# Kernel tuning notes

Hardware: AMD Instinct MI355X
Metric: run time of the kernel (lower is better)

## Reference

```python
import jax, jax.numpy as jnp
import numpy as np

NUM_HEADS = 16
D_MODEL = 1024
DEPTH = D_MODEL // NUM_HEADS
B, S = 4, 1024  # q,k seq len = S; v seq len = S-1


def setup_inputs() -> dict:
    key = jax.random.key(0)
    ks = jax.random.split(key, 6)
    scale = 1.0 / np.sqrt(D_MODEL)
    return {
        "v": jax.random.normal(ks[0], (B, S - 1, D_MODEL), dtype=jnp.float32),
        "k": jax.random.normal(ks[1], (B, S, D_MODEL), dtype=jnp.float32),
        "q": jax.random.normal(ks[2], (B, S, D_MODEL), dtype=jnp.float32),
        "mask": jnp.zeros((B, S - 1, S - 1), dtype=jnp.float32),
        "Wv": jax.random.normal(ks[3], (D_MODEL, D_MODEL), dtype=jnp.float32) * scale,
        "bv": jnp.zeros((D_MODEL,), dtype=jnp.float32),
        "Wd": jax.random.normal(ks[4], (D_MODEL, D_MODEL), dtype=jnp.float32) * scale,
        "bd": jnp.zeros((D_MODEL,), dtype=jnp.float32),
    }


def _split_heads(x):
    # (B, T, d_model) -> (B, H, T, depth)
    b, t, _ = x.shape
    return x.reshape(b, t, NUM_HEADS, DEPTH).transpose(0, 2, 1, 3)


def reference(v, k, q, mask, Wv, bv, Wd, bd):
    # 3-D q/k path: qq=q, kk=k (q_layers/k_layers/wq/wk unused)
    vv = v @ Wv + bv                       # (B, S-1, d_model)
    qh = _split_heads(q)                   # (B, H, S, depth)
    kh = _split_heads(k)                   # (B, H, S, depth)
    vh = _split_heads(vv)                  # (B, H, S-1, depth)

    scores = jnp.einsum('bhqd,bhkd->bhqk', qh, kh)      # (B, H, S, S)
    scores = scores[:, :, 1:, :-1]                      # (B, H, S-1, S-1)
    dk = jnp.asarray(DEPTH, scores.dtype)
    nl = jax.nn.relu(scores / jnp.sqrt(dk))
    nl = nl + mask[:, None, :, :] * (-1e9)
    att = jax.nn.softmax(nl, axis=-1)                   # (B, H, S-1, S-1)

    out = jnp.einsum('bhqk,bhkd->bhqd', att, vh)        # (B, H, S-1, depth)
    out = out.transpose(0, 2, 1, 3).reshape(v.shape[0], -1, D_MODEL)  # (B, S-1, d_model)
    output = out @ Wd + bd
    return output, att
```

## Files before the change

### kernel.cpp

```cpp
#include <hip/hip_runtime.h>
#include <hip/hip_bf16.h>

#define NUM_HEADS 16
#define DM 1024
#define DEPTH 64
#define BB 4
#define SS 1024
#define SL 1023
#define M_ROWS (BB*SL)

typedef __attribute__((ext_vector_type(8))) short short8;
typedef __attribute__((ext_vector_type(4))) float floatx4;

__device__ inline unsigned short f2bf(float f) {
  __hip_bfloat16 hb = __float2bfloat16(f);
  return *reinterpret_cast<unsigned short*>(&hb);
}
__device__ inline short8 ld_frag(const unsigned short* p) {
  return *reinterpret_cast<const short8*>(p);
}

template <bool A_BF16, bool OUT_BF16>
__global__ __launch_bounds__(256) void gemm_bias(
    const void* __restrict__ Av, const float* __restrict__ B,
    const float* __restrict__ bias, void* __restrict__ Cv, int M)
{
  __shared__ unsigned short bshT[128][40];
  const int tid = threadIdx.x;
  const int w = tid >> 6, lane = tid & 63, q4 = lane >> 4, l16 = lane & 15;
  const int wm = w >> 1, wn = w & 1;
  const int rb = blockIdx.y * 128 + wm * 64;
  const int cb = blockIdx.x * 128;
  const int wc = wn * 64;

  floatx4 acc[4][4];
  #pragma unroll
  for (int i = 0; i < 4; i++)
    #pragma unroll
    for (int j = 0; j < 4; j++) acc[i][j] = (floatx4){0.f,0.f,0.f,0.f};

  const int sn = tid & 127;
  const int sk = (tid >> 7) * 16;

  for (int k0 = 0; k0 < DM; k0 += 32) {
    __syncthreads();
    {
      const float* bp = B + (size_t)(k0 + sk) * DM + cb + sn;
      unsigned short tmp[16];
      #pragma unroll
      for (int j = 0; j < 16; j++) tmp[j] = f2bf(bp[(size_t)j * DM]);
      *(uint4*)&bshT[sn][sk]     = *(uint4*)&tmp[0];
      *(uint4*)&bshT[sn][sk + 8] = *(uint4*)&tmp[8];
    }
    __syncthreads();

    short8 af[4];
    #pragma unroll
    for (int i = 0; i < 4; i++) {
      int m = rb + i * 16 + l16;
      if (m < M) {
        if (A_BF16) {
          af[i] = ld_frag((const unsigned short*)Av + (size_t)m * DM + k0 + q4 * 8);
        } else {
          const float* ap = (const float*)Av + (size_t)m * DM + k0 + q4 * 8;
          float4 f0 = *(const float4*)ap;
          float4 f1 = *(const float4*)(ap + 4);
          short8 t;
          t[0]=f2bf(f0.x); t[1]=f2bf(f0.y); t[2]=f2bf(f0.z); t[3]=f2bf(f0.w);
          t[4]=f2bf(f1.x); t[5]=f2bf(f1.y); t[6]=f2bf(f1.z); t[7]=f2bf(f1.w);
          af[i] = t;
        }
      } else {
        af[i] = (short8){0,0,0,0,0,0,0,0};
      }
    }
    #pragma unroll
    for (int jn = 0; jn < 4; jn++) {
      short8 bf = ld_frag(&bshT[wc + jn * 16 + l16][q4 * 8]);
      #pragma unroll
      for (int i = 0; i < 4; i++)
        acc[i][jn] = __builtin_amdgcn_mfma_f32_16x16x32_bf16(af[i], bf, acc[i][jn], 0, 0, 0);
    }
  }

  #pragma unroll
  for (int jn = 0; jn < 4; jn++) {
    int col = cb + wc + jn * 16 + l16;
    float bb = bias[col];
    #pragma unroll
    for (int i = 0; i < 4; i++) {
      #pragma unroll
      for (int r = 0; r < 4; r++) {
        int m = rb + i * 16 + q4 * 4 + r;
        if (m < M) {
          float val = acc[i][jn][r] + bb;
          if (OUT_BF16) ((unsigned short*)Cv)[(size_t)m * DM + col] = f2bf(val);
          else          ((float*)Cv)[(size_t)m * DM + col] = val;
        }
      }
    }
  }
}

__global__ __launch_bounds__(256) void attn_kernel(
    const float* __restrict__ Q, const float* __restrict__ Kg,
    const float* __restrict__ Mask, const unsigned short* __restrict__ VV,
    float* __restrict__ Att, unsigned short* __restrict__ Out2)
{
  const int qt = blockIdx.x, h = blockIdx.y, b = blockIdx.z;
  const int tid = threadIdx.x;
  const int w = tid >> 6, lane = tid & 63, q4 = lane >> 4, l16 = lane & 15;
  const int qi0 = qt * 64;
  const int qb = w * 16;

  __shared__ unsigned short qsh[64][72];
  __shared__ unsigned short ksh[64][72];
  __shared__ unsigned short vshT[64][72];
  __shared__ unsigned short psh[4][16][72];

  {
    int qr = tid >> 2, d0 = (tid & 3) * 16;
    int qi = qi0 + qr;
    unsigned short tmp[16];
    if (qi < SL) {
      const float* src = Q + ((size_t)b * SS + qi + 1) * DM + h * DEPTH + d0;
      #pragma unroll
      for (int j = 0; j < 16; j += 4) {
        float4 f = *(const float4*)(src + j);
        tmp[j+0]=f2bf(f.x); tmp[j+1]=f2bf(f.y); tmp[j+2]=f2bf(f.z); tmp[j+3]=f2bf(f.w);
      }
    } else {
      #pragma unroll
      for (int j = 0; j < 16; j++) tmp[j] = 0;
    }
    *(uint4*)&qsh[qr][d0]     = *(uint4*)&tmp[0];
    *(uint4*)&qsh[qr][d0 + 8] = *(uint4*)&tmp[8];
  }

  auto stageK = [&](int kt) {
    int kr = tid >> 2, d0 = (tid & 3) * 16;
    int kj = kt * 64 + kr;
    unsigned short tmp[16];
    if (kj < SL) {
      const float* src = Kg + ((size_t)b * SS + kj) * DM + h * DEPTH + d0;
      #pragma unroll
      for (int j = 0; j < 16; j += 4) {
        float4 f = *(const float4*)(src + j);
        tmp[j+0]=f2bf(f.x); tmp[j+1]=f2bf(f.y); tmp[j+2]=f2bf(f.z); tmp[j+3]=f2bf(f.w);
      }
    } else {
      #pragma unroll
      for (int j = 0; j < 16; j++) tmp[j] = 0;
    }
    *(uint4*)&ksh[kr][d0]     = *(uint4*)&tmp[0];
    *(uint4*)&ksh[kr][d0 + 8] = *(uint4*)&tmp[8];
  };

  auto stageV = [&](int kt) {
    int d = tid & 63, k16 = (tid >> 6) * 16;
    unsigned short tmp[16];
    #pragma unroll
    for (int j = 0; j < 16; j++) {
      int kj = kt * 64 + k16 + j;
      tmp[j] = (kj < SL) ? VV[((size_t)b * SL + kj) * DM + h * DEPTH + d] : (unsigned short)0;
    }
    *(uint4*)&vshT[d][k16]     = *(uint4*)&tmp[0];
    *(uint4*)&vshT[d][k16 + 8] = *(uint4*)&tmp[8];
  };

  __syncthreads();

  float rsv[4] = {0.f, 0.f, 0.f, 0.f};
  for (int kt = 0; kt < 16; kt++) {
    __syncthreads();
    stageK(kt);
    __syncthreads();
    #pragma unroll
    for (int nt = 0; nt < 4; nt++) {
      floatx4 s = (floatx4){0.f,0.f,0.f,0.f};
      s = __builtin_amdgcn_mfma_f32_16x16x32_bf16(
            ld_frag(&qsh[qb + l16][q4*8]), ld_frag(&ksh[nt*16 + l16][q4*8]), s, 0,0,0);
      s = __builtin_amdgcn_mfma_f32_16x16x32_bf16(
            ld_frag(&qsh[qb + l16][32 + q4*8]), ld_frag(&ksh[nt*16 + l16][32 + q4*8]), s, 0,0,0);
      int kj = kt * 64 + nt * 16 + l16;
      bool kv = kj < SL;
      int qi_b = qi0 + qb + q4 * 4;
      const float* mp = Mask + ((size_t)b * SL + qi_b) * SL + kj;
      #pragma unroll
      for (int r = 0; r < 4; r++) {
        int qi = qi_b + r;
        float mval = (kv && qi < SL) ? mp[(size_t)r * SL] : 0.f;
        float sv = fmaxf(s[r] * 0.125f, 0.f) + mval * (-1e9f);
        float p = kv ? __expf(sv) : 0.f;
        rsv[r] += p;
      }
    }
  }
  #pragma unroll
  for (int r = 0; r < 4; r++) {
    #pragma unroll
    for (int off = 1; off < 16; off <<= 1) rsv[r] += __shfl_xor(rsv[r], off, 64);
  }
  float inv[4];
  #pragma unroll
  for (int r = 0; r < 4; r++) inv[r] = 1.f / rsv[r];

  floatx4 oacc[4];
  #pragma unroll
  for (int i = 0; i < 4; i++) oacc[i] = (floatx4){0.f,0.f,0.f,0.f};

  for (int kt = 0; kt < 16; kt++) {
    __syncthreads();
    stageK(kt);
    stageV(kt);
    __syncthreads();
    #pragma unroll
    for (int nt = 0; nt < 4; nt++) {
      floatx4 s = (floatx4){0.f,0.f,0.f,0.f};
      s = __builtin_amdgcn_mfma_f32_16x16x32_bf16(
            ld_frag(&qsh[qb + l16][q4*8]), ld_frag(&ksh[nt*16 + l16][q4*8]), s, 0,0,0);
      s = __builtin_amdgcn_mfma_f32_16x16x32_bf16(
            ld_frag(&qsh[qb + l16][32 + q4*8]), ld_frag(&ksh[nt*16 + l16][32 + q4*8]), s, 0,0,0);
      int kj = kt * 64 + nt * 16 + l16;
      bool kv = kj < SL;
      int qi_b = qi0 + qb + q4 * 4;
      const float* mp = Mask + ((size_t)b * SL + qi_b) * SL + kj;
      #pragma unroll
      for (int r = 0; r < 4; r++) {
        int qi = qi_b + r;
        bool qv = qi < SL;
        float mval = (kv && qv) ? mp[(size_t)r * SL] : 0.f;
        float sv = fmaxf(s[r] * 0.125f, 0.f) + mval * (-1e9f);
        float p = kv ? __expf(sv) : 0.f;
        float pn = p * inv[r];
        if (kv && qv)
          Att[(((size_t)(b * NUM_HEADS + h)) * SL + qi) * SL + kj] = pn;
        psh[w][q4 * 4 + r][nt * 16 + l16] = f2bf(pn);
      }
    }
    short8 pa0 = ld_frag(&psh[w][l16][q4 * 8]);
    short8 pa1 = ld_frag(&psh[w][l16][32 + q4 * 8]);
    #pragma unroll
    for (int nt2 = 0; nt2 < 4; nt2++) {
      oacc[nt2] = __builtin_amdgcn_mfma_f32_16x16x32_bf16(
                    pa0, ld_frag(&vshT[nt2*16 + l16][q4*8]), oacc[nt2], 0,0,0);
      oacc[nt2] = __builtin_amdgcn_mfma_f32_16x16x32_bf16(
                    pa1, ld_frag(&vshT[nt2*16 + l16][32 + q4*8]), oacc[nt2], 0,0,0);
    }
  }

  #pragma unroll
  for (int nt2 = 0; nt2 < 4; nt2++) {
    #pragma unroll
    for (int r = 0; r < 4; r++) {
      int qi = qi0 + qb + q4 * 4 + r;
      if (qi < SL)
        Out2[((size_t)b * SL + qi) * DM + h * DEPTH + nt2 * 16 + l16] = f2bf(oacc[nt2][r]);
    }
  }
}

extern "C" void kernel_launch(void* const* d_in, const int* in_sizes, int n_in,
                              void* d_out, int out_size, void* d_ws, size_t ws_size,
                              hipStream_t stream) {
  const float* v    = (const float*)d_in[0];
  const float* k    = (const float*)d_in[1];
  const float* q    = (const float*)d_in[2];
  const float* mask = (const float*)d_in[3];
  const float* Wv   = (const float*)d_in[4];
  const float* bv   = (const float*)d_in[5];
  const float* Wd   = (const float*)d_in[6];
  const float* bd   = (const float*)d_in[7];

  float* out = (float*)d_out;
  float* att = out + (size_t)M_ROWS * DM;
  unsigned short* vv   = (unsigned short*)d_ws;
  unsigned short* out2 = vv + (size_t)M_ROWS * DM;

  gemm_bias<false, true><<<dim3(DM/128, (M_ROWS+127)/128), 256, 0, stream>>>(
      (const void*)v, Wv, bv, (void*)vv, M_ROWS);
  attn_kernel<<<dim3(16, NUM_HEADS, BB), 256, 0, stream>>>(q, k, mask, vv, att, out2);
  gemm_bias<true, false><<<dim3(DM/128, (M_ROWS+127)/128), 256, 0, stream>>>(
      (const void*)out2, Wd, bd, (void*)out, M_ROWS);
}
```

Baseline: 782.5 us.

## Pre-convert operands to bf16 and double-buffer GEMM tiles via global_load_lds

Adds separate kernels that convert v to bf16 and write transposed bf16 copies of Wv and Wd. The GEMMs then stream both operands into swizzled, double-buffered LDS with direct global-to-LDS loads. This replaces the per-iteration strided fp32 weight loads and in-loop conversions with a smaller 64x128 tile. Scratch buffers borrow the att output area and the vv workspace, which relies on the launch order to stay correct, and the extra launches and conversion passes add memory traffic.

New measurement: 667.0 us. 14.8% less time.

```diff
diff --git a/kernel.cpp b/kernel.cpp
--- a/kernel.cpp
+++ b/kernel.cpp
@@ -20,80 +20,138 @@
   return *reinterpret_cast<const short8*>(p);
 }
 
-template <bool A_BF16, bool OUT_BF16>
-__global__ __launch_bounds__(256) void gemm_bias(
-    const void* __restrict__ Av, const float* __restrict__ B,
-    const float* __restrict__ bias, void* __restrict__ Cv, int M)
+#define GLDS(g, l) __builtin_amdgcn_global_load_lds( \
+    (const __attribute__((address_space(1))) void*)(g), \
+    (__attribute__((address_space(3))) void*)(l), 16, 0, 0)
+
+__global__ __launch_bounds__(256) void f32_to_bf16_vec(
+    const float* __restrict__ in, unsigned short* __restrict__ out, int n8)
 {
-  __shared__ unsigned short bshT[128][40];
+  int i = blockIdx.x * 256 + threadIdx.x;
+  if (i >= n8) return;
+  const float4 f0 = ((const float4*)in)[(size_t)i * 2];
+  const float4 f1 = ((const float4*)in)[(size_t)i * 2 + 1];
+  unsigned short t[8];
+  t[0]=f2bf(f0.x); t[1]=f2bf(f0.y); t[2]=f2bf(f0.z); t[3]=f2bf(f0.w);
+  t[4]=f2bf(f1.x); t[5]=f2bf(f1.y); t[6]=f2bf(f1.z); t[7]=f2bf(f1.w);
+  ((uint4*)out)[i] = *(uint4*)t;
+}
+
+__global__ __launch_bounds__(256) void transpose_to_bf16(
+    const float* __restrict__ W, unsigned short* __restrict__ WT)
+{
+  __shared__ unsigned short tile[64][72];
+  const int tid = threadIdx.x;
+  const int k0 = blockIdx.y * 64, n0 = blockIdx.x * 64;
+  {
+    const int kl = tid >> 2, nc = (tid & 3) * 16;
+    const float* src = W + (size_t)(k0 + kl) * DM + n0 + nc;
+    #pragma unroll
+    for (int j = 0; j < 16; j += 4) {
+      float4 f = *(const float4*)(src + j);
+      tile[nc + j + 0][kl] = f2bf(f.x);
+      tile[nc + j + 1][kl] = f2bf(f.y);
+      tile[nc + j + 2][kl] = f2bf(f.z);
+      tile[nc + j + 3][kl] = f2bf(f.w);
+    }
+  }
+  __syncthreads();
+  {
+    const int nl = tid >> 2, kc = (tid & 3) * 16;
+    unsigned short tmp[16];
+    #pragma unroll
+    for (int j = 0; j < 16; j++) tmp[j] = tile[nl][kc + j];
+    unsigned short* dst = WT + (size_t)(n0 + nl) * DM + k0 + kc;
+    *(uint4*)&dst[0] = *(uint4*)&tmp[0];
+    *(uint4*)&dst[8] = *(uint4*)&tmp[8];
+  }
+}
+
+template <bool OUT_BF16>
+__global__ __launch_bounds__(256) void gemm_bt(
+    const unsigned short* __restrict__ A,
+    const unsigned short* __restrict__ BT,
+    const float* __restrict__ bias,
+    void* __restrict__ Cv, int M)
+{
+  constexpr int BM = 64, BN = 128, BK = 32;
+  __shared__ __align__(16) unsigned short As[2][BM * BK];
+  __shared__ __align__(16) unsigned short Bs[2][BN * BK];
+
   const int tid = threadIdx.x;
   const int w = tid >> 6, lane = tid & 63, q4 = lane >> 4, l16 = lane & 15;
   const int wm = w >> 1, wn = w & 1;
-  const int rb = blockIdx.y * 128 + wm * 64;
-  const int cb = blockIdx.x * 128;
-  const int wc = wn * 64;
-
-  floatx4 acc[4][4];
-  #pragma unroll
-  for (int i = 0; i < 4; i++)
+  const int rb = blockIdx.y * BM;
+  const int cb = blockIdx.x * BN;
+
+  const int a_row = tid >> 2;
+  const int a_slot = (tid & 3) ^ ((a_row >> 1) & 3);
+  int a_grow = rb + a_row; if (a_grow >= M) a_grow = M - 1;
+  const unsigned short* a_src = A + (size_t)a_grow * DM + a_slot * 8;
+  const int b_row0 = tid >> 2;
+  const int b_row1 = 64 + (tid >> 2);
+  const int b_slot0 = (tid & 3) ^ ((b_row0 >> 1) & 3);
+  const int b_slot1 = (tid & 3) ^ ((b_row1 >> 1) & 3);
+  const unsigned short* b_src0 = BT + (size_t)(cb + b_row0) * DM + b_slot0 * 8;
+  const unsigned short* b_src1 = BT + (size_t)(cb + b_row1) * DM + b_slot1 * 8;
+
+  int aoff[2], boff[4];
+  #pragma unroll
+  for (int i = 0; i < 2; i++) {
+    int r = wm * 32 + i * 16 + l16;
+    aoff[i] = r * BK + ((q4 ^ ((r >> 1) & 3)) * 8);
+  }
+  #pragma unroll
+  for (int j = 0; j < 4; j++) {
+    int r = wn * 64 + j * 16 + l16;
+    boff[j] = r * BK + ((q4 ^ ((r >> 1) & 3)) * 8);
+  }
+
+  floatx4 acc[2][4];
+  #pragma unroll
+  for (int i = 0; i < 2; i++)
     #pragma unroll
     for (int j = 0; j < 4; j++) acc[i][j] = (floatx4){0.f,0.f,0.f,0.f};
 
-  const int sn = tid & 127;
-  const int sk = (tid >> 7) * 16;
-
-  for (int k0 = 0; k0 < DM; k0 += 32) {
-    __syncthreads();
-    {
-      const float* bp = B + (size_t)(k0 + sk) * DM + cb + sn;
-      unsigned short tmp[16];
-      #pragma unroll
-      for (int j = 0; j < 16; j++) tmp[j] = f2bf(bp[(size_t)j * DM]);
-      *(uint4*)&bshT[sn][sk]     = *(uint4*)&tmp[0];
-      *(uint4*)&bshT[sn][sk + 8] = *(uint4*)&tmp[8];
-    }
-    __syncthreads();
-
-    short8 af[4];
-    #pragma unroll
-    for (int i = 0; i < 4; i++) {
-      int m = rb + i * 16 + l16;
-      if (m < M) {
-        if (A_BF16) {
-          af[i] = ld_frag((const unsigned short*)Av + (size_t)m * DM + k0 + q4 * 8);
-        } else {
-          const float* ap = (const float*)Av + (size_t)m * DM + k0 + q4 * 8;
-          float4 f0 = *(const float4*)ap;
-          float4 f1 = *(const float4*)(ap + 4);
-          short8 t;
-          t[0]=f2bf(f0.x); t[1]=f2bf(f0.y); t[2]=f2bf(f0.z); t[3]=f2bf(f0.w);
-          t[4]=f2bf(f1.x); t[5]=f2bf(f1.y); t[6]=f2bf(f1.z); t[7]=f2bf(f1.w);
-          af[i] = t;
-        }
-      } else {
-        af[i] = (short8){0,0,0,0,0,0,0,0};
-      }
-    }
-    #pragma unroll
-    for (int jn = 0; jn < 4; jn++) {
-      short8 bf = ld_frag(&bshT[wc + jn * 16 + l16][q4 * 8]);
-      #pragma unroll
-      for (int i = 0; i < 4; i++)
-        acc[i][jn] = __builtin_amdgcn_mfma_f32_16x16x32_bf16(af[i], bf, acc[i][jn], 0, 0, 0);
-    }
-  }
-
-  #pragma unroll
-  for (int jn = 0; jn < 4; jn++) {
-    int col = cb + wc + jn * 16 + l16;
+  GLDS(a_src,  &As[0][tid * 8]);
+  GLDS(b_src0, &Bs[0][tid * 8]);
+  GLDS(b_src1, &Bs[0][2048 + tid * 8]);
+  __syncthreads();
+
+  int cur = 0;
+  constexpr int NT = DM / BK;
+  for (int t = 0; t < NT; ++t) {
+    if (t + 1 < NT) {
+      const int kn = (t + 1) * BK;
+      GLDS(a_src + kn,  &As[cur ^ 1][tid * 8]);
+      GLDS(b_src0 + kn, &Bs[cur ^ 1][tid * 8]);
+      GLDS(b_src1 + kn, &Bs[cur ^ 1][2048 + tid * 8]);
+    }
+    short8 af[2], bfr[4];
+    #pragma unroll
+    for (int i = 0; i < 2; i++) af[i] = ld_frag(&As[cur][aoff[i]]);
+    #pragma unroll
+    for (int j = 0; j < 4; j++) bfr[j] = ld_frag(&Bs[cur][boff[j]]);
+    #pragma unroll
+    for (int i = 0; i < 2; i++)
+      #pragma unroll
+      for (int j = 0; j < 4; j++)
+        acc[i][j] = __builtin_amdgcn_mfma_f32_16x16x32_bf16(af[i], bfr[j], acc[i][j], 0, 0, 0);
+    __syncthreads();
+    cur ^= 1;
+  }
+
+  #pragma unroll
+  for (int j = 0; j < 4; j++) {
+    int col = cb + wn * 64 + j * 16 + l16;
     float bb = bias[col];
     #pragma unroll
-    for (int i = 0; i < 4; i++) {
+    for (int i = 0; i < 2; i++) {
       #pragma unroll
       for (int r = 0; r < 4; r++) {
-        int m = rb + i * 16 + q4 * 4 + r;
+        int m = rb + wm * 32 + i * 16 + q4 * 4 + r;
         if (m < M) {
-          float val = acc[i][jn][r] + bb;
+          float val = acc[i][j][r] + bb;
           if (OUT_BF16) ((unsigned short*)Cv)[(size_t)m * DM + col] = f2bf(val);
           else          ((float*)Cv)[(size_t)m * DM + col] = val;
         }
@@ -277,9 +335,16 @@
   unsigned short* vv   = (unsigned short*)d_ws;
   unsigned short* out2 = vv + (size_t)M_ROWS * DM;
 
-  gemm_bias<false, true><<<dim3(DM/128, (M_ROWS+127)/128), 256, 0, stream>>>(
-      (const void*)v, Wv, bv, (void*)vv, M_ROWS);
+  unsigned short* WvT = (unsigned short*)att;
+  unsigned short* vbf = WvT + (size_t)DM * DM;
+  unsigned short* WdT = vv;
+
+  const int n8 = (M_ROWS * DM) / 8;
+
+  f32_to_bf16_vec<<<dim3((n8 + 255) / 256), 256, 0, stream>>>(v, vbf, n8);
+  transpose_to_bf16<<<dim3(16, 16), 256, 0, stream>>>(Wv, WvT);
+  gemm_bt<true><<<dim3(DM/128, (M_ROWS+63)/64), 256, 0, stream>>>(vbf, WvT, bv, (void*)vv, M_ROWS);
   attn_kernel<<<dim3(16, NUM_HEADS, BB), 256, 0, stream>>>(q, k, mask, vv, att, out2);
-  gemm_bias<true, false><<<dim3(DM/128, (M_ROWS+127)/128), 256, 0, stream>>>(
-      (const void*)out2, Wd, bd, (void*)out, M_ROWS);
-}
+  transpose_to_bf16<<<dim3(16, 16), 256, 0, stream>>>(Wd, WdT);
+  gemm_bt<false><<<dim3(DM/128, (M_ROWS+63)/64), 256, 0, stream>>>(out2, WdT, bd, (void*)out, M_ROWS);
+}
```
